# Kernel optimization log

Hardware: AMD Instinct MI355X
Metric: run time of the kernel (lower is better)

Reference implementation:

```python
import jax, jax.numpy as jnp
import numpy as np

B, T, D_IN, D_HID, D_OUT, N_CAT = 128, 64, 1024, 1024, 1536, 32


def setup_inputs() -> dict:
    key = jax.random.key(0)
    kx, kw1, kw2, kc = jax.random.split(key, 4)
    x = jax.random.normal(kx, (B, T, D_IN), dtype=jnp.float32)
    W1 = 0.02 * jax.random.normal(kw1, (N_CAT, D_IN, D_HID), dtype=jnp.float32)
    b1 = jnp.zeros((N_CAT, D_HID), dtype=jnp.float32)
    W2 = 0.02 * jax.random.normal(kw2, (N_CAT, D_HID, D_OUT), dtype=jnp.float32)
    b2 = jnp.zeros((N_CAT, D_OUT), dtype=jnp.float32)
    cat_ids = jax.random.randint(kc, (B,), 0, N_CAT)
    return {"x": x, "W1": W1, "b1": b1, "W2": W2, "b2": b2, "cat_ids": cat_ids}


def reference(x, W1, b1, W2, b2, cat_ids):
    # CategorySpecificLinear: gather per-sample expert weights, then batched matmul.
    # Layer 1: (B,T,D_in) @ (B,D_in,D_hid) + (B,1,D_hid)
    h = jnp.einsum('btd,bdh->bth', x, W1[cat_ids]) + b1[cat_ids][:, None, :]
    h = jax.nn.relu(h)
    # Layer 2: (B,T,D_hid) @ (B,D_hid,D_out) + (B,1,D_out)
    out = jnp.einsum('bth,bho->bto', h, W2[cat_ids]) + b2[cat_ids][:, None, :]
    return out
```

## Files before the change

kernel.cpp:

```cpp
#include <hip/hip_runtime.h>
#include <hip/hip_bf16.h>
#include <stdint.h>

#define NB    128
#define TT    64
#define KTOT  1024
#define DHID  1024
#define DOUT  1536
#define NCAT  32

#define BK    64
#define TN    128
#define PADR  72

typedef unsigned short u16;
typedef __attribute__((ext_vector_type(8))) short bf16x8;
typedef __attribute__((ext_vector_type(4))) float f32x4;
typedef __attribute__((ext_vector_type(4))) unsigned int uint4v;
typedef __attribute__((ext_vector_type(4))) float float4v;

__device__ __forceinline__ float bf2f(u16 u) {
    unsigned int x = ((unsigned int)u) << 16;
    return __builtin_bit_cast(float, x);
}
__device__ __forceinline__ unsigned int f2bf_u32(float f) {
    unsigned int x = __builtin_bit_cast(unsigned int, f);
    return (x + 0x7FFFu + ((x >> 16) & 1u)) >> 16;
}
__device__ __forceinline__ u16 f2bf(float f) { return (u16)f2bf_u32(f); }

__device__ int g_is_f32;

__global__ void detect_dtype(const unsigned int* __restrict__ xw) {
    if (threadIdx.x == 0 && blockIdx.x == 0) {
        int hits = 0;
        for (int i = 0; i < 256; ++i) {
            unsigned int e = (xw[i] >> 7) & 0xFF;
            hits += (e >= 120 && e <= 132) ? 1 : 0;
        }
        g_is_f32 = (hits < 128) ? 1 : 0;
    }
}

template<int NW, bool RELU, bool A_DYN, bool OUT_DYN>
__global__ __launch_bounds__(256, 4)
void gemm_cat(const void* __restrict__ Ain,
              const void* __restrict__ Win,
              const void* __restrict__ BiasIn,
              void* __restrict__ Cout,
              const int* __restrict__ cat_ids)
{
    constexpr int NT = NW / TN;
    __shared__ u16 As[TT * PADR];
    __shared__ u16 Bs[TN * PADR];

    const bool f32  = (g_is_f32 != 0);
    const bool aF32 = A_DYN && f32;
    const bool oF32 = OUT_DYN && f32;

    const int b   = blockIdx.x / NT;
    const int nt  = blockIdx.x % NT;
    const int cat = cat_ids[b];

    const int tid  = threadIdx.x;
    const int lane = tid & 63;
    const int l16  = lane & 15;
    const int q    = lane >> 4;
    const int wave = tid >> 6;
    const int wm   = wave & 1;
    const int wn   = wave >> 1;

    const size_t aOff = (size_t)b * (TT * KTOT);
    const u16*   Ab16 = (const u16*)Ain + aOff;
    const float* Ab32 = (const float*)Ain + aOff;
    const size_t wOff = (size_t)cat * ((size_t)KTOT * NW) + (size_t)nt * TN;
    const u16*   Wb16 = (const u16*)Win + wOff;
    const float* Wb32 = (const float*)Win + wOff;

    const int ar = tid >> 2;
    const int ac = (tid & 3) * 16;
    const int bn  = tid & 127;
    const int bk0 = tid >> 7;

    f32x4 acc[2][4];
#pragma unroll
    for (int im = 0; im < 2; ++im)
#pragma unroll
        for (int in = 0; in < 4; ++in)
            acc[im][in] = (f32x4){0.f, 0.f, 0.f, 0.f};

    for (int kk = 0; kk < KTOT; kk += BK) {
        if (!aF32) {
            const u16* src = Ab16 + ar * KTOT + kk + ac;
            uint4v v0 = *(const uint4v*)(src);
            uint4v v1 = *(const uint4v*)(src + 8);
            *(uint4v*)&As[ar * PADR + ac]     = v0;
            *(uint4v*)&As[ar * PADR + ac + 8] = v1;
        } else {
            const float* src = Ab32 + ar * KTOT + kk + ac;
            float4v f0 = *(const float4v*)(src);
            float4v f1 = *(const float4v*)(src + 4);
            float4v f2 = *(const float4v*)(src + 8);
            float4v f3 = *(const float4v*)(src + 12);
            uint4v v0, v1;
            v0.x = f2bf_u32(f0.x) | (f2bf_u32(f0.y) << 16);
            v0.y = f2bf_u32(f0.z) | (f2bf_u32(f0.w) << 16);
            v0.z = f2bf_u32(f1.x) | (f2bf_u32(f1.y) << 16);
            v0.w = f2bf_u32(f1.z) | (f2bf_u32(f1.w) << 16);
            v1.x = f2bf_u32(f2.x) | (f2bf_u32(f2.y) << 16);
            v1.y = f2bf_u32(f2.z) | (f2bf_u32(f2.w) << 16);
            v1.z = f2bf_u32(f3.x) | (f2bf_u32(f3.y) << 16);
            v1.w = f2bf_u32(f3.z) | (f2bf_u32(f3.w) << 16);
            *(uint4v*)&As[ar * PADR + ac]     = v0;
            *(uint4v*)&As[ar * PADR + ac + 8] = v1;
        }
#pragma unroll
        for (int i = 0; i < 4; ++i) {
            const int kc = bk0 + i * 2;
            unsigned int s[8];
            if (!f32) {
                const u16* src = Wb16 + (size_t)(kk + kc * 8) * NW + bn;
#pragma unroll
                for (int j = 0; j < 8; ++j) s[j] = src[(size_t)j * NW];
            } else {
                const float* src = Wb32 + (size_t)(kk + kc * 8) * NW + bn;
#pragma unroll
                for (int j = 0; j < 8; ++j) s[j] = f2bf_u32(src[(size_t)j * NW]);
            }
            uint4v v;
            v.x = s[0] | (s[1] << 16);
            v.y = s[2] | (s[3] << 16);
            v.z = s[4] | (s[5] << 16);
            v.w = s[6] | (s[7] << 16);
            *(uint4v*)&Bs[bn * PADR + kc * 8] = v;
        }
        __syncthreads();

#pragma unroll
        for (int s = 0; s < 2; ++s) {
            bf16x8 a[2], bb[4];
#pragma unroll
            for (int im = 0; im < 2; ++im)
                a[im] = *(const bf16x8*)&As[(wm * 32 + im * 16 + l16) * PADR + s * 32 + q * 8];
#pragma unroll
            for (int in = 0; in < 4; ++in)
                bb[in] = *(const bf16x8*)&Bs[(wn * 64 + in * 16 + l16) * PADR + s * 32 + q * 8];
#pragma unroll
            for (int im = 0; im < 2; ++im)
#pragma unroll
                for (int in = 0; in < 4; ++in)
                    acc[im][in] = __builtin_amdgcn_mfma_f32_16x16x32_bf16(
                        a[im], bb[in], acc[im][in], 0, 0, 0);
        }
        __syncthreads();
    }

    const u16*   bias16 = (const u16*)BiasIn + (size_t)cat * NW + nt * TN;
    const float* bias32 = (const float*)BiasIn + (size_t)cat * NW + nt * TN;
    const size_t cOff = (size_t)b * TT * NW + (size_t)nt * TN;
    u16*   C16 = (u16*)Cout + cOff;
    float* C32 = (float*)Cout + cOff;
#pragma unroll
    for (int in = 0; in < 4; ++in) {
        const int ncol = wn * 64 + in * 16 + l16;
        const float bv = f32 ? bias32[ncol] : bf2f(bias16[ncol]);
#pragma unroll
        for (int im = 0; im < 2; ++im) {
#pragma unroll
            for (int r = 0; r < 4; ++r) {
                const int m = wm * 32 + im * 16 + q * 4 + r;
                float v = acc[im][in][r] + bv;
                if (RELU) v = fmaxf(v, 0.f);
                if (oF32) C32[(size_t)m * NW + ncol] = v;
                else      C16[(size_t)m * NW + ncol] = f2bf(v);
            }
        }
    }
}

extern "C" void kernel_launch(void* const* d_in, const int* in_sizes, int n_in,
                              void* d_out, int out_size, void* d_ws, size_t ws_size,
                              hipStream_t stream) {
    const void* x   = d_in[0];
    const void* W1  = d_in[1];
    const void* b1  = d_in[2];
    const void* W2  = d_in[3];
    const void* b2  = d_in[4];
    const int*  cid = (const int*)d_in[5];

    u16* h = (u16*)d_ws;

    detect_dtype<<<1, 64, 0, stream>>>((const unsigned int*)x);
    gemm_cat<DHID, true,  true,  false><<<NB * (DHID / TN), 256, 0, stream>>>(
        x, W1, b1, (void*)h, cid);
    gemm_cat<DOUT, false, false, true ><<<NB * (DOUT / TN), 256, 0, stream>>>(
        (const void*)h, W2, b2, d_out, cid);
}
```

Measured before the change: 561.6 us.

## Pre-transpose weights to bf16 K-major and load via direct-to-LDS with swizzle

```diff
diff --git a/kernel.cpp b/kernel.cpp
--- a/kernel.cpp
+++ b/kernel.cpp
@@ -11,7 +11,6 @@
 
 #define BK    64
 #define TN    128
-#define PADR  72
 
 typedef unsigned short u16;
 typedef __attribute__((ext_vector_type(8))) short bf16x8;
@@ -42,13 +41,184 @@
     }
 }
 
+template<int NW>
+__global__ __launch_bounds__(256)
+void transpose_w(const void* __restrict__ Win, u16* __restrict__ WT)
+{
+    constexpr int NBLK = NW / 256;
+    const bool f32 = (g_is_f32 != 0);
+    const int cat  = blockIdx.x / (16 * NBLK);
+    const int rem  = blockIdx.x % (16 * NBLK);
+    const int kb   = rem / NBLK;
+    const int nb   = rem % NBLK;
+
+    const int n  = nb * 256 + threadIdx.x;
+    const int k0 = kb * 64;
+
+    const size_t srcOff = (size_t)cat * ((size_t)KTOT * NW);
+    const u16*   s16 = (const u16*)Win + srcOff;
+    const float* s32 = (const float*)Win + srcOff;
+    u16* dst = WT + ((size_t)cat * NW + n) * KTOT + k0;
+
+#pragma unroll
+    for (int j = 0; j < 8; ++j) {
+        unsigned int s[8];
+        if (!f32) {
+#pragma unroll
+            for (int i = 0; i < 8; ++i)
+                s[i] = s16[(size_t)(k0 + j * 8 + i) * NW + n];
+        } else {
+#pragma unroll
+            for (int i = 0; i < 8; ++i)
+                s[i] = f2bf_u32(s32[(size_t)(k0 + j * 8 + i) * NW + n]);
+        }
+        uint4v v;
+        v.x = s[0] | (s[1] << 16);
+        v.y = s[2] | (s[3] << 16);
+        v.z = s[4] | (s[5] << 16);
+        v.w = s[6] | (s[7] << 16);
+        *(uint4v*)(dst + j * 8) = v;
+    }
+}
+
 template<int NW, bool RELU, bool A_DYN, bool OUT_DYN>
 __global__ __launch_bounds__(256, 4)
-void gemm_cat(const void* __restrict__ Ain,
-              const void* __restrict__ Win,
-              const void* __restrict__ BiasIn,
-              void* __restrict__ Cout,
-              const int* __restrict__ cat_ids)
+void gemm_fast(const void* __restrict__ Ain,
+               const u16* __restrict__ WT,
+               const void* __restrict__ BiasIn,
+               void* __restrict__ Cout,
+               const int* __restrict__ cat_ids)
+{
+    constexpr int NT = NW / TN;
+    __shared__ u16 As[TT * BK];
+    __shared__ u16 Ws[TN * BK];
+
+    const bool f32  = (g_is_f32 != 0);
+    const bool aF32 = A_DYN && f32;
+    const bool oF32 = OUT_DYN && f32;
+
+    const int b   = blockIdx.x / NT;
+    const int nt  = blockIdx.x % NT;
+    const int cat = cat_ids[b];
+
+    const int tid  = threadIdx.x;
+    const int lane = tid & 63;
+    const int l16  = lane & 15;
+    const int q    = lane >> 4;
+    const int wave = tid >> 6;
+    const int wm   = wave & 1;
+    const int wn   = wave >> 1;
+
+    const size_t aOff = (size_t)b * (TT * KTOT);
+    const u16*   Ab16 = (const u16*)Ain + aOff;
+    const float* Ab32 = (const float*)Ain + aOff;
+    const u16* Wt = WT + (size_t)cat * ((size_t)NW * KTOT) + (size_t)(nt * TN) * KTOT;
+
+    const int ar = tid >> 2;
+    const int c0 = (tid & 3) * 2;
+    const int p0 = c0 ^ (ar & 7);
+    const int p1 = (c0 + 1) ^ (ar & 7);
+    const int lrow = lane >> 3;
+    const int lc   = (lane & 7) ^ lrow;
+
+    f32x4 acc[2][4];
+#pragma unroll
+    for (int im = 0; im < 2; ++im)
+#pragma unroll
+        for (int in = 0; in < 4; ++in)
+            acc[im][in] = (f32x4){0.f, 0.f, 0.f, 0.f};
+
+    for (int kk = 0; kk < KTOT; kk += BK) {
+#pragma unroll
+        for (int j = 0; j < 4; ++j) {
+            const int row = wave * 32 + j * 8 + lrow;
+            const u16* g = Wt + (size_t)row * KTOT + kk + lc * 8;
+            __builtin_amdgcn_global_load_lds(
+                (const __attribute__((address_space(1))) void*)g,
+                (__attribute__((address_space(3))) void*)&Ws[(wave * 4 + j) * 512],
+                16, 0, 0);
+        }
+        if (!aF32) {
+            const u16* src = Ab16 + ar * KTOT + kk + c0 * 8;
+            uint4v v0 = *(const uint4v*)(src);
+            uint4v v1 = *(const uint4v*)(src + 8);
+            *(uint4v*)&As[ar * BK + p0 * 8] = v0;
+            *(uint4v*)&As[ar * BK + p1 * 8] = v1;
+        } else {
+            const float* src = Ab32 + ar * KTOT + kk + c0 * 8;
+            float4v f0 = *(const float4v*)(src);
+            float4v f1 = *(const float4v*)(src + 4);
+            float4v f2 = *(const float4v*)(src + 8);
+            float4v f3 = *(const float4v*)(src + 12);
+            uint4v v0, v1;
+            v0.x = f2bf_u32(f0.x) | (f2bf_u32(f0.y) << 16);
+            v0.y = f2bf_u32(f0.z) | (f2bf_u32(f0.w) << 16);
+            v0.z = f2bf_u32(f1.x) | (f2bf_u32(f1.y) << 16);
+            v0.w = f2bf_u32(f1.z) | (f2bf_u32(f1.w) << 16);
+            v1.x = f2bf_u32(f2.x) | (f2bf_u32(f2.y) << 16);
+            v1.y = f2bf_u32(f2.z) | (f2bf_u32(f2.w) << 16);
+            v1.z = f2bf_u32(f3.x) | (f2bf_u32(f3.y) << 16);
+            v1.w = f2bf_u32(f3.z) | (f2bf_u32(f3.w) << 16);
+            *(uint4v*)&As[ar * BK + p0 * 8] = v0;
+            *(uint4v*)&As[ar * BK + p1 * 8] = v1;
+        }
+        __syncthreads();
+
+#pragma unroll
+        for (int s = 0; s < 2; ++s) {
+            const int c = s * 4 + q;
+            bf16x8 a[2], bb[4];
+#pragma unroll
+            for (int im = 0; im < 2; ++im) {
+                const int r = wm * 32 + im * 16 + l16;
+                a[im] = *(const bf16x8*)&As[r * BK + (c ^ (l16 & 7)) * 8];
+            }
+#pragma unroll
+            for (int in = 0; in < 4; ++in) {
+                const int r = wn * 64 + in * 16 + l16;
+                bb[in] = *(const bf16x8*)&Ws[r * BK + (c ^ (l16 & 7)) * 8];
+            }
+#pragma unroll
+            for (int im = 0; im < 2; ++im)
+#pragma unroll
+                for (int in = 0; in < 4; ++in)
+                    acc[im][in] = __builtin_amdgcn_mfma_f32_16x16x32_bf16(
+                        a[im], bb[in], acc[im][in], 0, 0, 0);
+        }
+        __syncthreads();
+    }
+
+    const u16*   bias16 = (const u16*)BiasIn + (size_t)cat * NW + nt * TN;
+    const float* bias32 = (const float*)BiasIn + (size_t)cat * NW + nt * TN;
+    const size_t cOff = (size_t)b * TT * NW + (size_t)nt * TN;
+    u16*   C16 = (u16*)Cout + cOff;
+    float* C32 = (float*)Cout + cOff;
+#pragma unroll
+    for (int in = 0; in < 4; ++in) {
+        const int ncol = wn * 64 + in * 16 + l16;
+        const float bv = f32 ? bias32[ncol] : bf2f(bias16[ncol]);
+#pragma unroll
+        for (int im = 0; im < 2; ++im) {
+#pragma unroll
+            for (int r = 0; r < 4; ++r) {
+                const int m = wm * 32 + im * 16 + q * 4 + r;
+                float v = acc[im][in][r] + bv;
+                if (RELU) v = fmaxf(v, 0.f);
+                if (oF32) C32[(size_t)m * NW + ncol] = v;
+                else      C16[(size_t)m * NW + ncol] = f2bf(v);
+            }
+        }
+    }
+}
+
+#define PADR  72
+template<int NW, bool RELU, bool A_DYN, bool OUT_DYN>
+__global__ __launch_bounds__(256, 4)
+void gemm_cat_v2(const void* __restrict__ Ain,
+                 const void* __restrict__ Win,
+                 const void* __restrict__ BiasIn,
+                 void* __restrict__ Cout,
+                 const int* __restrict__ cat_ids)
 {
     constexpr int NT = NW / TN;
     __shared__ u16 As[TT * PADR];
@@ -135,7 +305,6 @@
             *(uint4v*)&Bs[bn * PADR + kc * 8] = v;
         }
         __syncthreads();
-
 #pragma unroll
         for (int s = 0; s < 2; ++s) {
             bf16x8 a[2], bb[4];
@@ -188,11 +357,26 @@
     const void* b2  = d_in[4];
     const int*  cid = (const int*)d_in[5];
 
+    const size_t hBytes   = (size_t)NB * TT * DHID * sizeof(u16);
+    const size_t w1tBytes = (size_t)NCAT * KTOT * DHID * sizeof(u16);
+    const size_t w2tBytes = (size_t)NCAT * KTOT * DOUT * sizeof(u16);
     u16* h = (u16*)d_ws;
 
     detect_dtype<<<1, 64, 0, stream>>>((const unsigned int*)x);
-    gemm_cat<DHID, true,  true,  false><<<NB * (DHID / TN), 256, 0, stream>>>(
-        x, W1, b1, (void*)h, cid);
-    gemm_cat<DOUT, false, false, true ><<<NB * (DOUT / TN), 256, 0, stream>>>(
-        (const void*)h, W2, b2, d_out, cid);
-}
+
+    if (ws_size >= hBytes + w1tBytes + w2tBytes) {
+        u16* W1T = (u16*)((char*)d_ws + hBytes);
+        u16* W2T = (u16*)((char*)d_ws + hBytes + w1tBytes);
+        transpose_w<DHID><<<NCAT * 16 * (DHID / 256), 256, 0, stream>>>(W1, W1T);
+        transpose_w<DOUT><<<NCAT * 16 * (DOUT / 256), 256, 0, stream>>>(W2, W2T);
+        gemm_fast<DHID, true,  true,  false><<<NB * (DHID / TN), 256, 0, stream>>>(
+            x, W1T, b1, (void*)h, cid);
+        gemm_fast<DOUT, false, false, true ><<<NB * (DOUT / TN), 256, 0, stream>>>(
+            (const void*)h, W2T, b2, d_out, cid);
+    } else {
+        gemm_cat_v2<DHID, true,  true,  false><<<NB * (DHID / TN), 256, 0, stream>>>(
+            x, W1, b1, (void*)h, cid);
+        gemm_cat_v2<DOUT, false, false, true ><<<NB * (DOUT / TN), 256, 0, stream>>>(
+            (const void*)h, W2, b2, d_out, cid);
+    }
+}
```

Measured after the change: 690.2 us. +22.9%, slower.
